# Optimization experiments

Hardware: AMD Instinct MI355X
Metric: run time of the kernel (lower is better)

Reference implementation:

```python
import jax, jax.numpy as jnp
import numpy as np

ALPHA = 1.5
BETA = 0.5
AVG_RATIO = 1.0
SUM_TIMESTEPS = 28000
RANK = 8
K_TOP = RANK * RANK  # k = weight_1_a.shape[1] * weight_2_a.shape[1]


def setup_inputs() -> dict:
    key = jax.random.key(0)
    ks = jax.random.split(key, 5)
    B, S, D_IN, D_OUT = 2, 4096, 4096, 4096
    return {
        "hidden_states": jax.random.normal(ks[0], (B, S, D_IN), dtype=jnp.float32),
        "weight_1_a": jax.random.normal(ks[1], (D_OUT, RANK), dtype=jnp.float32) * 0.02,
        "weight_1_b": jax.random.normal(ks[2], (RANK, D_IN), dtype=jnp.float32) * 0.02,
        "weight_2_a": jax.random.normal(ks[3], (D_OUT, RANK), dtype=jnp.float32) * 0.02,
        "weight_2_b": jax.random.normal(ks[4], (RANK, D_IN), dtype=jnp.float32) * 0.02,
        "timestep": 1,
    }


def reference(hidden_states, weight_1_a, weight_1_b, weight_2_a, weight_2_b, timestep):
    # Low-rank expansions: [out, rank] @ [rank, in] -> [out, in]
    matrix1 = weight_1_a @ weight_1_b
    matrix2 = weight_2_a @ weight_2_b
    top_k_sum1 = jax.lax.top_k(jnp.abs(matrix1).ravel(), K_TOP)[0].sum()
    top_k_sum2 = jax.lax.top_k(jnp.abs(matrix2).ravel(), K_TOP)[0].sum()
    time_ratio = timestep % SUM_TIMESTEPS
    scale = (ALPHA * time_ratio / SUM_TIMESTEPS + BETA) % ALPHA  # pattern 's*'
    temp_ratio = (top_k_sum1 / AVG_RATIO) / (top_k_sum2 * scale)
    weight = jnp.where(temp_ratio > 1.0, matrix1, matrix2)  # [out, in]
    # F.linear: x @ W^T
    return jnp.einsum("bsi,oi->bso", hidden_states, weight)
```

## Files before the change

### kernel.cpp

```cpp
#include <hip/hip_runtime.h>
#include <stdint.h>

#define D 4096
#define RANK 8
#define ALPHA 1.5f
#define BETA 0.5f
#define SUM_TIMESTEPS 28000
#define K_TOP 64
#define NBINS 1024

typedef float f32x4 __attribute__((ext_vector_type(4)));

#define WS_GCNT_OFF 256
#define WS_GSUM_OFF (256 + 2 * NBINS * 4)
#define WS_BMAX_OFF (WS_GSUM_OFF + 2 * NBINS * 8)

#define FIX_NUM 2.74877906944e11f
#define FIX_INV 3.637978807091713e-12

__device__ __forceinline__ float dot4v(f32x4 a, f32x4 b) {
    return fmaf(a.x, b.x, fmaf(a.y, b.y, fmaf(a.z, b.z, a.w * b.w)));
}

__global__ __launch_bounds__(256) void k_pass_max(
    const float* __restrict__ wa1, const float* __restrict__ wb1,
    const float* __restrict__ wa2, const float* __restrict__ wb2,
    unsigned* __restrict__ gz, unsigned* __restrict__ bmax) {
    const int tid = threadIdx.x;
    const int mat = blockIdx.y;
    const int bid = blockIdx.x;
    if (mat == 0 && tid < 24) gz[bid * 24 + tid] = 0u;

    const float* __restrict__ wa = mat ? wa2 : wa1;
    const float* __restrict__ wb = mat ? wb2 : wb1;
    const int i0 = (bid & 3) * 1024 + tid * 4;
    const int obase = (bid >> 2) * 64;

    __shared__ float was[64][8];
    if (tid < 128)
        ((f32x4*)was)[tid] = ((const f32x4*)(wa + (size_t)obase * RANK))[tid];

    f32x4 wbv[RANK];
#pragma unroll
    for (int r = 0; r < RANK; ++r)
        wbv[r] = *(const f32x4*)(wb + r * D + i0);
    __syncthreads();

    float vmax = 0.f;
#pragma unroll 4
    for (int oo = 0; oo < 64; ++oo) {
        const f32x4 w03 = *(const f32x4*)&was[oo][0];
        const f32x4 w47 = *(const f32x4*)&was[oo][4];
        f32x4 s = {0.f, 0.f, 0.f, 0.f};
        const float a[8] = {w03.x, w03.y, w03.z, w03.w, w47.x, w47.y, w47.z, w47.w};
#pragma unroll
        for (int r = 0; r < RANK; ++r) {
            s.x = fmaf(a[r], wbv[r].x, s.x);
            s.y = fmaf(a[r], wbv[r].y, s.y);
            s.z = fmaf(a[r], wbv[r].z, s.z);
            s.w = fmaf(a[r], wbv[r].w, s.w);
        }
        vmax = fmaxf(vmax, fmaxf(fmaxf(fabsf(s.x), fabsf(s.y)),
                                 fmaxf(fabsf(s.z), fabsf(s.w))));
    }
    for (int off = 32; off; off >>= 1)
        vmax = fmaxf(vmax, __shfl_xor(vmax, off, 64));
    __shared__ float smax[4];
    const int wave = tid >> 6, lane = tid & 63;
    if (lane == 0) smax[wave] = vmax;
    __syncthreads();
    if (tid == 0) {
        float m = fmaxf(fmaxf(smax[0], smax[1]), fmaxf(smax[2], smax[3]));
        bmax[mat * 256 + bid] = __float_as_uint(m);
    }
}

__device__ __forceinline__ float block_max256(const unsigned* __restrict__ bmax,
                                              int mat, int tid, float* redm) {
    const int wave = tid >> 6, lane = tid & 63;
    float m = 0.f;
    if (tid < 256) m = __uint_as_float(bmax[mat * 256 + tid]);
    for (int off = 32; off; off >>= 1)
        m = fmaxf(m, __shfl_xor(m, off, 64));
    if (tid < 256 && lane == 0) redm[wave] = m;
    __syncthreads();
    return fmaxf(fmaxf(redm[0], redm[1]), fmaxf(redm[2], redm[3]));
}

__global__ __launch_bounds__(256) void k_pass_hist(
    const float* __restrict__ wa1, const float* __restrict__ wb1,
    const float* __restrict__ wa2, const float* __restrict__ wb2,
    const unsigned* __restrict__ bmax,
    unsigned* __restrict__ gcnt, unsigned long long* __restrict__ gsum) {
    __shared__ unsigned lcnt[NBINS];
    __shared__ unsigned long long lsum[NBINS];
    __shared__ float was[64][8];
    __shared__ float redm[4];
    const int tid = threadIdx.x;
    const int mat = blockIdx.y;
    for (int b = tid; b < NBINS; b += 256) { lcnt[b] = 0u; lsum[b] = 0ull; }

    const float* __restrict__ wa = mat ? wa2 : wa1;
    const float* __restrict__ wb = mat ? wb2 : wb1;
    const int i0 = (blockIdx.x & 3) * 1024 + tid * 4;
    const int obase = (blockIdx.x >> 2) * 64;
    if (tid < 128)
        ((f32x4*)was)[tid] = ((const f32x4*)(wa + (size_t)obase * RANK))[tid];

    const float M = block_max256(bmax, mat, tid, redm);
    const float T = 0.5f * M;
    const float fix = FIX_NUM / M;
    const unsigned bitsT = __float_as_uint(T);

    f32x4 wbv[RANK];
#pragma unroll
    for (int r = 0; r < RANK; ++r)
        wbv[r] = *(const f32x4*)(wb + r * D + i0);

#pragma unroll 2
    for (int oo = 0; oo < 64; ++oo) {
        const f32x4 w03 = *(const f32x4*)&was[oo][0];
        const f32x4 w47 = *(const f32x4*)&was[oo][4];
        f32x4 s = {0.f, 0.f, 0.f, 0.f};
        const float a[8] = {w03.x, w03.y, w03.z, w03.w, w47.x, w47.y, w47.z, w47.w};
#pragma unroll
        for (int r = 0; r < RANK; ++r) {
            s.x = fmaf(a[r], wbv[r].x, s.x);
            s.y = fmaf(a[r], wbv[r].y, s.y);
            s.z = fmaf(a[r], wbv[r].z, s.z);
            s.w = fmaf(a[r], wbv[r].w, s.w);
        }
        const float av[4] = {fabsf(s.x), fabsf(s.y), fabsf(s.z), fabsf(s.w)};
#pragma unroll
        for (int j = 0; j < 4; ++j) {
            if (av[j] >= T) {
                unsigned k = (__float_as_uint(av[j]) - bitsT) >> 13;
                if (k > NBINS - 1u) k = NBINS - 1u;
                atomicAdd(&lcnt[k], 1u);
                atomicAdd(&lsum[k], (unsigned long long)(av[j] * fix));
            }
        }
    }
    __syncthreads();
    unsigned* __restrict__ gc = gcnt + (size_t)mat * NBINS;
    unsigned long long* __restrict__ gs = gsum + (size_t)mat * NBINS;
    for (int b = tid; b < NBINS; b += 256) {
        unsigned c = lcnt[b];
        if (c) {
            atomicAdd(&gc[b], c);
            atomicAdd(&gs[b], lsum[b]);
        }
    }
}

__global__ __launch_bounds__(1024) void k_select(
    unsigned* __restrict__ hdr, const unsigned* __restrict__ bmax,
    const unsigned* __restrict__ gcnt, const unsigned long long* __restrict__ gsum,
    const int* __restrict__ tsp) {
    __shared__ unsigned sc[NBINS];
    __shared__ unsigned long long ss[NBINS];
    __shared__ float res[2];
    __shared__ float Ms[2];
    __shared__ float redm[4];
    __shared__ int sB;
    const int b = threadIdx.x;

    for (int mat = 0; mat < 2; ++mat) {
        float M = block_max256(bmax, mat, b, redm);
        if (b == 0) Ms[mat] = M;
        __syncthreads();
    }

    for (int mat = 0; mat < 2; ++mat) {
        if (b == 0) sB = -1;
        const unsigned c0 = gcnt[(size_t)mat * NBINS + b];
        const unsigned long long s0 = gsum[(size_t)mat * NBINS + b];
        __syncthreads();
        sc[b] = c0;
        ss[b] = s0;
        __syncthreads();
        for (int step = 1; step < NBINS; step <<= 1) {
            unsigned c2 = 0u; unsigned long long s2 = 0ull;
            if (b + step < NBINS) { c2 = sc[b + step]; s2 = ss[b + step]; }
            __syncthreads();
            sc[b] += c2;
            ss[b] += s2;
            __syncthreads();
        }
        if (sc[b] >= K_TOP && (b == NBINS - 1 || sc[b + 1] < K_TOP)) sB = b;
        __syncthreads();
        if (b == 0) {
            const double inv = (double)Ms[mat] * FIX_INV;
            float total;
            if (sB < 0) {
                total = (float)((double)ss[0] * inv);
            } else {
                const int B = sB;
                const unsigned cAbove = (B + 1 < NBINS) ? sc[B + 1] : 0u;
                const unsigned long long sAbove = (B + 1 < NBINS) ? ss[B + 1] : 0ull;
                const unsigned cb = sc[B] - cAbove;
                const unsigned long long sb = ss[B] - sAbove;
                const unsigned need = K_TOP - cAbove;
                total = (float)((double)sAbove * inv)
                      + (float)((double)sb * inv) * ((float)need / (float)cb);
            }
            res[mat] = total;
        }
        __syncthreads();
    }
    if (b == 0) {
        const int tr = (*tsp) % SUM_TIMESTEPS;
        const float scale = fmodf(ALPHA * (float)tr / (float)SUM_TIMESTEPS + BETA, ALPHA);
        const float temp_ratio = res[0] / (res[1] * scale);
        hdr[4] = (temp_ratio > 1.0f) ? 1u : 0u;
    }
}

__global__ __launch_bounds__(256) void k_fused(
    const float* __restrict__ h,
    const float* __restrict__ wa1, const float* __restrict__ wb1,
    const float* __restrict__ wa2, const float* __restrict__ wb2,
    const unsigned* __restrict__ hdr,
    float* __restrict__ out) {
    const int tid = threadIdx.x;
    const int wave = tid >> 6, lane = tid & 63;
    const unsigned flag = hdr[4];
    const float* __restrict__ wa = flag ? wa1 : wa2;
    const float* __restrict__ wb = flag ? wb1 : wb2;
    const size_t m0 = (size_t)blockIdx.x * 16;
    const int r0w = wave * 4;

    __shared__ float wbs[RANK][1024];
    __shared__ float ts[16][8];

    float acc[4][RANK];
#pragma unroll
    for (int row = 0; row < 4; ++row)
#pragma unroll
        for (int r = 0; r < RANK; ++r) acc[row][r] = 0.f;

    const f32x4* __restrict__ src = (const f32x4*)wb;
    f32x4* __restrict__ dst = (f32x4*)wbs;

    for (int q = 0; q < 4; ++q) {
        __syncthreads();
        f32x4 sreg[8];
#pragma unroll
        for (int t = 0; t < 8; ++t) {
            const int j = t * 256 + tid;
            sreg[t] = src[(j >> 8) * 1024 + q * 256 + (j & 255)];
        }
        f32x4 hv[4][4];
#pragma unroll
        for (int k = 0; k < 4; ++k)
#pragma unroll
            for (int row = 0; row < 4; ++row)
                hv[k][row] = *(const f32x4*)(h + (m0 + r0w + row) * D
                                             + q * 1024 + k * 256 + lane * 4);
#pragma unroll
        for (int t = 0; t < 8; ++t) dst[t * 256 + tid] = sreg[t];
        __syncthreads();
#pragma unroll
        for (int k = 0; k < 4; ++k) {
            const int il = k * 256 + lane * 4;
            f32x4 wbv[RANK];
#pragma unroll
            for (int r = 0; r < RANK; ++r)
                wbv[r] = *(const f32x4*)&wbs[r][il];
#pragma unroll
            for (int row = 0; row < 4; ++row)
#pragma unroll
                for (int r = 0; r < RANK; ++r)
                    acc[row][r] = fmaf(hv[k][row].x, wbv[r].x,
                                  fmaf(hv[k][row].y, wbv[r].y,
                                  fmaf(hv[k][row].z, wbv[r].z,
                                  fmaf(hv[k][row].w, wbv[r].w, acc[row][r]))));
        }
    }

#pragma unroll
    for (int row = 0; row < 4; ++row)
#pragma unroll
        for (int r = 0; r < RANK; ++r)
#pragma unroll
            for (int off = 32; off; off >>= 1)
                acc[row][r] += __shfl_xor(acc[row][r], off, 64);
    if (lane == 0) {
#pragma unroll
        for (int row = 0; row < 4; ++row)
#pragma unroll
            for (int r = 0; r < RANK; ++r)
                ts[r0w + row][r] = acc[row][r];
    }
    __syncthreads();

    f32x4 A[8], An[8];
    {
        const int o0 = wave * 1024 + lane * 4;
#pragma unroll
        for (int j = 0; j < 8; ++j)
            A[j] = *(const f32x4*)(wa + (size_t)o0 * RANK + j * 4);
    }
    for (int cc = 0; cc < 4; ++cc) {
        if (cc < 3) {
            const int o1 = wave * 1024 + (cc + 1) * 256 + lane * 4;
#pragma unroll
            for (int j = 0; j < 8; ++j)
                An[j] = *(const f32x4*)(wa + (size_t)o1 * RANK + j * 4);
        }
        const int o0 = wave * 1024 + cc * 256 + lane * 4;
#pragma unroll 4
        for (int row = 0; row < 16; ++row) {
            const f32x4 t03 = *(const f32x4*)&ts[row][0];
            const f32x4 t47 = *(const f32x4*)&ts[row][4];
            f32x4 ov;
            ov.x = dot4v(A[0], t03) + dot4v(A[1], t47);
            ov.y = dot4v(A[2], t03) + dot4v(A[3], t47);
            ov.z = dot4v(A[4], t03) + dot4v(A[5], t47);
            ov.w = dot4v(A[6], t03) + dot4v(A[7], t47);
            __builtin_nontemporal_store(ov, (f32x4*)(out + (m0 + row) * D + o0));
        }
        if (cc < 3) {
#pragma unroll
            for (int j = 0; j < 8; ++j) A[j] = An[j];
        }
    }
}

extern "C" void kernel_launch(void* const* d_in, const int* in_sizes, int n_in,
                              void* d_out, int out_size, void* d_ws, size_t ws_size,
                              hipStream_t stream) {
    const float* h   = (const float*)d_in[0];
    const float* wa1 = (const float*)d_in[1];
    const float* wb1 = (const float*)d_in[2];
    const float* wa2 = (const float*)d_in[3];
    const float* wb2 = (const float*)d_in[4];
    const int*   ts  = (const int*)d_in[5];
    float* out = (float*)d_out;

    const int rows = in_sizes[0] / D;

    unsigned* hdr  = (unsigned*)d_ws;
    unsigned* gcnt = (unsigned*)((char*)d_ws + WS_GCNT_OFF);
    unsigned long long* gsum = (unsigned long long*)((char*)d_ws + WS_GSUM_OFF);
    unsigned* bmax = (unsigned*)((char*)d_ws + WS_BMAX_OFF);

    hipLaunchKernelGGL(k_pass_max, dim3(256, 2), dim3(256), 0, stream,
                       wa1, wb1, wa2, wb2, gcnt, bmax);
    hipLaunchKernelGGL(k_pass_hist, dim3(256, 2), dim3(256), 0, stream,
                       wa1, wb1, wa2, wb2, bmax, gcnt, gsum);
    hipLaunchKernelGGL(k_select, dim3(1), dim3(1024), 0, stream,
                       hdr, bmax, gcnt, gsum, ts);
    hipLaunchKernelGGL(k_fused, dim3(rows / 16), dim3(256), 0, stream,
                       h, wa1, wb1, wa2, wb2, hdr, out);
}
```

Baseline: 92.35 us.

## Split fused low-rank kernel into projection and expansion kernels

The fused kernel, which computed t = h @ Wb^T and then out = t @ Wa^T inside one block of 16 rows, is replaced by two kernels. The first computes t for 8 rows per block, which doubles the grid, and writes it to workspace. The second expands t into the output over 32 rows by a quarter of the columns per block, so more blocks can share the output-store bandwidth. This adds one kernel launch and a small round trip of t through global memory, and gives better occupancy and load balance in both phases.

```diff
diff --git a/kernel.cpp b/kernel.cpp
--- a/kernel.cpp
+++ b/kernel.cpp
@@ -14,6 +14,7 @@
 #define WS_GCNT_OFF 256
 #define WS_GSUM_OFF (256 + 2 * NBINS * 4)
 #define WS_BMAX_OFF (WS_GSUM_OFF + 2 * NBINS * 8)
+#define WS_T_OFF    (WS_BMAX_OFF + 2048)
 
 #define FIX_NUM 2.74877906944e11f
 #define FIX_INV 3.637978807091713e-12
@@ -216,26 +217,22 @@
     }
 }
 
-__global__ __launch_bounds__(256) void k_fused(
+__global__ __launch_bounds__(256) void k_t(
     const float* __restrict__ h,
-    const float* __restrict__ wa1, const float* __restrict__ wb1,
-    const float* __restrict__ wa2, const float* __restrict__ wb2,
+    const float* __restrict__ wb1, const float* __restrict__ wb2,
     const unsigned* __restrict__ hdr,
-    float* __restrict__ out) {
+    float* __restrict__ t) {
     const int tid = threadIdx.x;
     const int wave = tid >> 6, lane = tid & 63;
-    const unsigned flag = hdr[4];
-    const float* __restrict__ wa = flag ? wa1 : wa2;
-    const float* __restrict__ wb = flag ? wb1 : wb2;
-    const size_t m0 = (size_t)blockIdx.x * 16;
-    const int r0w = wave * 4;
+    const float* __restrict__ wb = hdr[4] ? wb1 : wb2;
+    const size_t m0 = (size_t)blockIdx.x * 8;
+    const int r0w = wave * 2;
 
     __shared__ float wbs[RANK][1024];
-    __shared__ float ts[16][8];
-
-    float acc[4][RANK];
-#pragma unroll
-    for (int row = 0; row < 4; ++row)
+
+    float acc[2][RANK];
+#pragma unroll
+    for (int row = 0; row < 2; ++row)
 #pragma unroll
         for (int r = 0; r < RANK; ++r) acc[row][r] = 0.f;
 
@@ -246,19 +243,19 @@
         __syncthreads();
         f32x4 sreg[8];
 #pragma unroll
-        for (int t = 0; t < 8; ++t) {
-            const int j = t * 256 + tid;
-            sreg[t] = src[(j >> 8) * 1024 + q * 256 + (j & 255)];
-        }
-        f32x4 hv[4][4];
+        for (int s = 0; s < 8; ++s) {
+            const int j = s * 256 + tid;
+            sreg[s] = src[(j >> 8) * 1024 + q * 256 + (j & 255)];
+        }
+        f32x4 hv[4][2];
 #pragma unroll
         for (int k = 0; k < 4; ++k)
 #pragma unroll
-            for (int row = 0; row < 4; ++row)
+            for (int row = 0; row < 2; ++row)
                 hv[k][row] = *(const f32x4*)(h + (m0 + r0w + row) * D
                                              + q * 1024 + k * 256 + lane * 4);
 #pragma unroll
-        for (int t = 0; t < 8; ++t) dst[t * 256 + tid] = sreg[t];
+        for (int s = 0; s < 8; ++s) dst[s * 256 + tid] = sreg[s];
         __syncthreads();
 #pragma unroll
         for (int k = 0; k < 4; ++k) {
@@ -268,7 +265,7 @@
             for (int r = 0; r < RANK; ++r)
                 wbv[r] = *(const f32x4*)&wbs[r][il];
 #pragma unroll
-            for (int row = 0; row < 4; ++row)
+            for (int row = 0; row < 2; ++row)
 #pragma unroll
                 for (int r = 0; r < RANK; ++r)
                     acc[row][r] = fmaf(hv[k][row].x, wbv[r].x,
@@ -279,7 +276,7 @@
     }
 
 #pragma unroll
-    for (int row = 0; row < 4; ++row)
+    for (int row = 0; row < 2; ++row)
 #pragma unroll
         for (int r = 0; r < RANK; ++r)
 #pragma unroll
@@ -287,43 +284,45 @@
                 acc[row][r] += __shfl_xor(acc[row][r], off, 64);
     if (lane == 0) {
 #pragma unroll
-        for (int row = 0; row < 4; ++row)
+        for (int row = 0; row < 2; ++row)
 #pragma unroll
             for (int r = 0; r < RANK; ++r)
-                ts[r0w + row][r] = acc[row][r];
-    }
-    __syncthreads();
-
-    f32x4 A[8], An[8];
-    {
-        const int o0 = wave * 1024 + lane * 4;
-#pragma unroll
-        for (int j = 0; j < 8; ++j)
-            A[j] = *(const f32x4*)(wa + (size_t)o0 * RANK + j * 4);
-    }
-    for (int cc = 0; cc < 4; ++cc) {
-        if (cc < 3) {
-            const int o1 = wave * 1024 + (cc + 1) * 256 + lane * 4;
-#pragma unroll
-            for (int j = 0; j < 8; ++j)
-                An[j] = *(const f32x4*)(wa + (size_t)o1 * RANK + j * 4);
-        }
-        const int o0 = wave * 1024 + cc * 256 + lane * 4;
+                t[(m0 + r0w + row) * RANK + r] = acc[row][r];
+    }
+}
+
+__global__ __launch_bounds__(256) void k_o(
+    const float* __restrict__ t,
+    const float* __restrict__ wa1, const float* __restrict__ wa2,
+    const unsigned* __restrict__ hdr,
+    float* __restrict__ out) {
+    const int tid = threadIdx.x;
+    const int wave = tid >> 6, lane = tid & 63;
+    const float* __restrict__ wa = hdr[4] ? wa1 : wa2;
+    const int cslice = blockIdx.x & 3;
+    const size_t m0 = (size_t)(blockIdx.x >> 2) * 32;
+    const int o0 = cslice * 1024 + wave * 256 + lane * 4;
+
+    __shared__ float ts[32][8];
+    if (tid < 64)
+        ((f32x4*)ts)[tid] = *(const f32x4*)(t + m0 * RANK + tid * 4);
+
+    f32x4 A[8];
+#pragma unroll
+    for (int j = 0; j < 8; ++j)
+        A[j] = *(const f32x4*)(wa + (size_t)o0 * RANK + j * 4);
+    __syncthreads();
+
 #pragma unroll 4
-        for (int row = 0; row < 16; ++row) {
-            const f32x4 t03 = *(const f32x4*)&ts[row][0];
-            const f32x4 t47 = *(const f32x4*)&ts[row][4];
-            f32x4 ov;
-            ov.x = dot4v(A[0], t03) + dot4v(A[1], t47);
-            ov.y = dot4v(A[2], t03) + dot4v(A[3], t47);
-            ov.z = dot4v(A[4], t03) + dot4v(A[5], t47);
-            ov.w = dot4v(A[6], t03) + dot4v(A[7], t47);
-            __builtin_nontemporal_store(ov, (f32x4*)(out + (m0 + row) * D + o0));
-        }
-        if (cc < 3) {
-#pragma unroll
-            for (int j = 0; j < 8; ++j) A[j] = An[j];
-        }
+    for (int row = 0; row < 32; ++row) {
+        const f32x4 t03 = *(const f32x4*)&ts[row][0];
+        const f32x4 t47 = *(const f32x4*)&ts[row][4];
+        f32x4 ov;
+        ov.x = dot4v(A[0], t03) + dot4v(A[1], t47);
+        ov.y = dot4v(A[2], t03) + dot4v(A[3], t47);
+        ov.z = dot4v(A[4], t03) + dot4v(A[5], t47);
+        ov.w = dot4v(A[6], t03) + dot4v(A[7], t47);
+        __builtin_nontemporal_store(ov, (f32x4*)(out + (m0 + row) * D + o0));
     }
 }
 
@@ -344,6 +343,7 @@
     unsigned* gcnt = (unsigned*)((char*)d_ws + WS_GCNT_OFF);
     unsigned long long* gsum = (unsigned long long*)((char*)d_ws + WS_GSUM_OFF);
     unsigned* bmax = (unsigned*)((char*)d_ws + WS_BMAX_OFF);
+    float*    tbuf = (float*)((char*)d_ws + WS_T_OFF);
 
     hipLaunchKernelGGL(k_pass_max, dim3(256, 2), dim3(256), 0, stream,
                        wa1, wb1, wa2, wb2, gcnt, bmax);
@@ -351,6 +351,8 @@
                        wa1, wb1, wa2, wb2, bmax, gcnt, gsum);
     hipLaunchKernelGGL(k_select, dim3(1), dim3(1024), 0, stream,
                        hdr, bmax, gcnt, gsum, ts);
-    hipLaunchKernelGGL(k_fused, dim3(rows / 16), dim3(256), 0, stream,
-                       h, wa1, wb1, wa2, wb2, hdr, out);
-}
+    hipLaunchKernelGGL(k_t, dim3(rows / 8), dim3(256), 0, stream,
+                       h, wb1, wb2, hdr, tbuf);
+    hipLaunchKernelGGL(k_o, dim3(4 * (rows / 32)), dim3(256), 0, stream,
+                       tbuf, wa1, wa2, hdr, out);
+}
```

Result: no change. 94.18 us (+2.0%).
